# Performance work log

Hardware: AMD Instinct MI355X
Metric: run time of the kernel (lower is better)

## Reference

```python
import jax, jax.numpy as jnp
import numpy as np

N = 4096
IN_DIM = 256
OUT_DIM = 256
NUM_HEADS = 4
HEAD_DIM = OUT_DIM // NUM_HEADS


def setup_inputs() -> dict:
    key = jax.random.key(0)
    ks = jax.random.split(key, 10)
    x = jax.random.normal(ks[0], (N, IN_DIM), dtype=jnp.float32)
    adj = jax.random.randint(ks[1], (N, N), 0, 2, dtype=jnp.int32)
    adj = jnp.maximum(adj, jnp.eye(N, dtype=jnp.int32))  # self-loops -> no empty rows
    s_in = 1.0 / np.sqrt(IN_DIM)
    s_out = 1.0 / np.sqrt(OUT_DIM)
    Wq = jax.random.uniform(ks[2], (IN_DIM, OUT_DIM), jnp.float32, -s_in, s_in)
    bq = jnp.zeros((OUT_DIM,), jnp.float32)
    Wk = jax.random.uniform(ks[3], (IN_DIM, OUT_DIM), jnp.float32, -s_in, s_in)
    bk = jnp.zeros((OUT_DIM,), jnp.float32)
    Wv = jax.random.uniform(ks[4], (IN_DIM, OUT_DIM), jnp.float32, -s_in, s_in)
    bv = jnp.zeros((OUT_DIM,), jnp.float32)
    Wo = jax.random.uniform(ks[5], (OUT_DIM, OUT_DIM), jnp.float32, -s_out, s_out)
    bo = jnp.zeros((OUT_DIM,), jnp.float32)
    gamma = jnp.ones((OUT_DIM,), jnp.float32)
    beta = jnp.zeros((OUT_DIM,), jnp.float32)
    return {"x": x, "adj": adj, "Wq": Wq, "bq": bq, "Wk": Wk, "bk": bk,
            "Wv": Wv, "bv": bv, "Wo": Wo, "bo": bo, "gamma": gamma, "beta": beta}


def layer_norm(h, gamma, beta, eps=1e-5):
    mu = jnp.mean(h, axis=-1, keepdims=True)
    var = jnp.mean(jnp.square(h - mu), axis=-1, keepdims=True)
    return (h - mu) * jax.lax.rsqrt(var + eps) * gamma + beta


def reference(x, adj, Wq, bq, Wk, bk, Wv, bv, Wo, bo, gamma, beta):
    n = x.shape[0]
    q_proj = x @ Wq + bq                       # (N, out_dim), reused for residual
    Q = q_proj.reshape(n, NUM_HEADS, HEAD_DIM)
    K = (x @ Wk + bk).reshape(n, NUM_HEADS, HEAD_DIM)
    V = (x @ Wv + bv).reshape(n, NUM_HEADS, HEAD_DIM)
    scores = jnp.einsum('nhd,mhd->nmh', Q, K) / np.sqrt(HEAD_DIM)
    scores = jnp.where(adj[:, :, None] == 0, -jnp.inf, scores)
    attn = jax.nn.softmax(scores, axis=1)      # softmax over neighbor axis m
    out = jnp.einsum('nmh,mhd->nhd', attn, V).reshape(n, OUT_DIM)
    out = out @ Wo + bo
    return layer_norm(out + q_proj, gamma, beta)
```

## Files before the change

### kernel.cpp

```cpp
#include <hip/hip_runtime.h>
#include <math.h>

#define NN 4096
#define DIM 256
#define NHEADS 4
#define HDIM 64

typedef short bf16x8 __attribute__((ext_vector_type(8)));
typedef float f32x4  __attribute__((ext_vector_type(4)));

__device__ __forceinline__ unsigned short f2bf(float f) {
    unsigned int u = __float_as_uint(f);
    u += 0x7fffu + ((u >> 16) & 1u);
    return (unsigned short)(u >> 16);
}
__device__ __forceinline__ float bf2f(unsigned short h) {
    return __uint_as_float(((unsigned int)h) << 16);
}
__device__ __forceinline__ void async16(const void* g, void* l) {
    __builtin_amdgcn_global_load_lds(
        (const __attribute__((address_space(1))) unsigned int*)g,
        (__attribute__((address_space(3))) unsigned int*)l, 16, 0, 0);
}

__global__ __launch_bounds__(256)
void prep_kernel(const float* __restrict__ W0, const float* __restrict__ W1,
                 const float* __restrict__ W2, const float* __restrict__ W3,
                 unsigned short* __restrict__ T0, unsigned short* __restrict__ T1,
                 unsigned short* __restrict__ T2, unsigned short* __restrict__ T3)
{
    __shared__ unsigned short Ts[64][65];
    const int b = blockIdx.x, t = threadIdx.x;
    const int mat = b >> 4, tile = b & 15;
    const int r0 = (tile >> 2) * 64, c0 = (tile & 3) * 64;
    const float* W = (mat == 0) ? W0 : (mat == 1) ? W1 : (mat == 2) ? W2 : W3;
    unsigned short* T = (mat == 0) ? T0 : (mat == 1) ? T1 : (mat == 2) ? T2 : T3;
    {
        int r = t >> 2, c4 = (t & 3) * 16;
        #pragma unroll
        for (int j = 0; j < 4; ++j) {
            float4 v = *reinterpret_cast<const float4*>(W + (size_t)(r0 + r) * DIM + c0 + c4 + j * 4);
            Ts[c4 + j * 4 + 0][r] = f2bf(v.x);
            Ts[c4 + j * 4 + 1][r] = f2bf(v.y);
            Ts[c4 + j * 4 + 2][r] = f2bf(v.z);
            Ts[c4 + j * 4 + 3][r] = f2bf(v.w);
        }
    }
    __syncthreads();
    {
        int d = t >> 2, k4 = (t & 3) * 16;
        #pragma unroll
        for (int j = 0; j < 4; ++j) {
            ushort4 u;
            u.x = Ts[d][k4 + j * 4 + 0];
            u.y = Ts[d][k4 + j * 4 + 1];
            u.z = Ts[d][k4 + j * 4 + 2];
            u.w = Ts[d][k4 + j * 4 + 3];
            *reinterpret_cast<ushort4*>(T + (size_t)(c0 + d) * DIM + r0 + k4 + j * 4) = u;
        }
    }
}

__global__ __launch_bounds__(256)
void qkv_mask(const float* __restrict__ x,
              const unsigned short* __restrict__ WqT, const unsigned short* __restrict__ WkT,
              const unsigned short* __restrict__ WvT,
              const float* __restrict__ bq, const float* __restrict__ bk, const float* __restrict__ bv,
              unsigned short* __restrict__ Qo, unsigned short* __restrict__ Ko,
              unsigned short* __restrict__ VTo,
              const int* __restrict__ adj, unsigned long long* __restrict__ maskT)
{
    const int b = blockIdx.x, t = threadIdx.x, w = t >> 6, l = t & 63;

    if (b >= 384) {
        const int ww = (b - 384) * 4 + w;
        for (int idx = ww; idx < 65536; idx += 8192) {
            const int row = idx >> 4, st = idx & 15;
            const int* ap = adj + (size_t)row * NN + st * 256 + l;
            const int a0 = ap[0];
            const int a1 = ap[64];
            const int a2 = ap[128];
            const int a3 = ap[192];
            unsigned long long b0 = __ballot(a0 != 0);
            unsigned long long b1 = __ballot(a1 != 0);
            unsigned long long b2 = __ballot(a2 != 0);
            unsigned long long b3 = __ballot(a3 != 0);
            if (l < 4) {
                unsigned long long bb = (l == 0) ? b0 : (l == 1) ? b1 : (l == 2) ? b2 : b3;
                maskT[(size_t)row * 64 + st * 4 + l] = bb;
            }
        }
        return;
    }

    const int l15 = l & 15, lg = l >> 4;
    const int which = b >> 7, xb = b & 127;
    const int row0 = xb * 32 + (w >> 1) * 16;
    const int col0 = (w & 1) * 128;
    const unsigned short* WT; const float* bias;
    if (which == 0)      { WT = WqT; bias = bq; }
    else if (which == 1) { WT = WkT; bias = bk; }
    else                 { WT = WvT; bias = bv; }

    f32x4 acc[8] = {};
    for (int k0 = 0; k0 < DIM; k0 += 32) {
        const float* xp = x + (size_t)(row0 + l15) * DIM + k0 + lg * 8;
        float4 x0 = *reinterpret_cast<const float4*>(xp);
        float4 x1 = *reinterpret_cast<const float4*>(xp + 4);
        union { unsigned u[4]; bf16x8 v; } xa;
        asm("v_cvt_pk_bf16_f32 %0, %1, %2" : "=v"(xa.u[0]) : "v"(x0.x), "v"(x0.y));
        asm("v_cvt_pk_bf16_f32 %0, %1, %2" : "=v"(xa.u[1]) : "v"(x0.z), "v"(x0.w));
        asm("v_cvt_pk_bf16_f32 %0, %1, %2" : "=v"(xa.u[2]) : "v"(x1.x), "v"(x1.y));
        asm("v_cvt_pk_bf16_f32 %0, %1, %2" : "=v"(xa.u[3]) : "v"(x1.z), "v"(x1.w));
        #pragma unroll
        for (int nt = 0; nt < 8; ++nt) {
            bf16x8 wb = *(const bf16x8*)(WT + (size_t)(col0 + nt * 16 + l15) * DIM + k0 + lg * 8);
            acc[nt] = __builtin_amdgcn_mfma_f32_16x16x32_bf16(xa.v, wb, acc[nt], 0, 0, 0);
        }
    }
    #pragma unroll
    for (int nt = 0; nt < 8; ++nt) {
        int col = col0 + nt * 16 + l15;
        float bb = bias[col];
        #pragma unroll
        for (int r = 0; r < 4; ++r) {
            int row = row0 + lg * 4 + r;
            float ov = acc[nt][r] + bb;
            if (which == 1) ov *= 0.18033688f;
            unsigned short val = f2bf(ov);
            if (which == 2) {
                int rb = row & 63;
                int vnt = rb >> 4, vlg = (rb >> 2) & 3, vr = rb & 3;
                int pos = ((vnt & 1) << 5) | (vlg << 3) | ((vnt >> 1) << 2) | vr;
                VTo[(size_t)col * NN + ((row & ~63) | pos)] = val;
            } else if (which == 0) Qo[(size_t)row * DIM + col] = val;
            else                   Ko[(size_t)row * DIM + col] = val;
        }
    }
}

template<int NTILES>
__global__ __launch_bounds__(256, 8)
void attn_mfma(const unsigned short* __restrict__ Qb, const unsigned short* __restrict__ Kb,
               const unsigned short* __restrict__ VT, const unsigned long long* __restrict__ maskT,
               unsigned short* __restrict__ Opart, float* __restrict__ lpart)
{
    constexpr int NSTR = NTILES / 4;
    __shared__ unsigned short Kt[2][64][64];
    __shared__ unsigned short Vt[2][64][64];

    const int t = threadIdx.x, w = t >> 6, l = t & 63, l15 = l & 15, lg = l >> 4;
    const int bid = blockIdx.x;
    const int slice = (bid & 7) + 8 * (bid >> 9);
    const int qb    = (bid >> 3) & 63;
    const int h  = slice & 3;
    const int sp = slice >> 2;
    const int n0 = qb * 64;
    const int kv_base = sp * NTILES * 64;
    const int qrow = n0 + w * 16;

    const unsigned short* qp = Qb + (size_t)(qrow + l15) * DIM + h * HDIM + lg * 8;
    const bf16x8 qa0 = *(const bf16x8*)(qp);
    const bf16x8 qa1 = *(const bf16x8*)(qp + 32);

    const unsigned long long* mbase = maskT + (size_t)(qrow + l15) * 64 + (kv_base >> 6);

    const int srow  = w * 16 + (l >> 3);
    const int sunit = (l & 7) ^ (srow & 7);
    const unsigned short* kS = Kb + (size_t)(kv_base + srow) * DIM + h * HDIM + sunit * 8;
    const unsigned short* vS = VT + (size_t)(h * HDIM + srow) * NN + kv_base + sunit * 8;

    const int xr  = l15 & 7;
    const int ko0 = (lg ^ xr) << 4;
    const int ko1 = ((4 + lg) ^ xr) << 4;

    const short onev = (l15 == 0) ? (short)0x3F80 : (short)0;
    const bf16x8 onesb = {onev, onev, onev, onev, onev, onev, onev, onev};

    f32x4 oa[4] = {};
    f32x4 os = {};

    {
        unsigned short* kd = &Kt[0][w * 16][0];
        unsigned short* vd = &Vt[0][w * 16][0];
        async16(kS, kd); async16(kS + 8 * DIM, kd + 8 * 64);
        async16(vS, vd); async16(vS + 8 * NN,  vd + 8 * 64);
    }

    #pragma unroll 1
    for (int st = 0; st < NSTR; ++st) {
        const ulonglong4 m4 = *reinterpret_cast<const ulonglong4*>(mbase + st * 4);

        #pragma unroll
        for (int m = 0; m < 4; ++m) {
            const int tl = st * 4 + m;
            asm volatile("s_waitcnt vmcnt(0)" ::: "memory");
            __builtin_amdgcn_s_barrier();
            __builtin_amdgcn_sched_barrier(0);

            if (tl + 1 < NTILES) {
                const int bb = (tl + 1) & 1;
                unsigned short* kd = &Kt[bb][w * 16][0];
                unsigned short* vd = &Vt[bb][w * 16][0];
                const unsigned short* ks = kS + (size_t)(tl + 1) * 64 * DIM;
                const unsigned short* vs = vS + (tl + 1) * 64;
                async16(ks, kd); async16(ks + 8 * DIM, kd + 8 * 64);
                async16(vs, vd); async16(vs + 8 * NN,  vd + 8 * 64);
            }

            const int cb = tl & 1;
            const char* kbase = (const char*)&Kt[cb][0][0] + l15 * 128;
            const char* vbase = (const char*)&Vt[cb][0][0] + l15 * 128;

            f32x4 sa[4] = {};
            __builtin_amdgcn_s_setprio(1);
            #pragma unroll
            for (int nt = 0; nt < 4; ++nt) {
                bf16x8 kb0 = *(const bf16x8*)(kbase + nt * 2048 + ko0);
                bf16x8 kb1 = *(const bf16x8*)(kbase + nt * 2048 + ko1);
                sa[nt] = __builtin_amdgcn_mfma_f32_16x16x32_bf16(kb0, qa0, sa[nt], 0, 0, 0);
                sa[nt] = __builtin_amdgcn_mfma_f32_16x16x32_bf16(kb1, qa1, sa[nt], 0, 0, 0);
            }
            __builtin_amdgcn_s_setprio(0);

            const unsigned long long w64 =
                (m == 0) ? m4.x : (m == 1) ? m4.y : (m == 2) ? m4.z : m4.w;
            const unsigned long long sh = w64 >> (lg * 4);
            const unsigned shlo = (unsigned)sh, shhi = (unsigned)(sh >> 32);
            float p[4][4];
            #pragma unroll
            for (int nt = 0; nt < 4; ++nt) {
                #pragma unroll
                for (int r = 0; r < 4; ++r) {
                    const int bitpos = nt * 16 + r;
                    const unsigned word = (bitpos < 32) ? shlo : shhi;
                    const unsigned bit = (word >> (bitpos & 31)) & 1u;
                    p[nt][r] = exp2f(bit ? sa[nt][r] : -INFINITY);
                }
            }
            union { unsigned u[4]; bf16x8 v; } a0, a1;
            asm("v_cvt_pk_bf16_f32 %0, %1, %2" : "=v"(a0.u[0]) : "v"(p[0][0]), "v"(p[0][1]));
            asm("v_cvt_pk_bf16_f32 %0, %1, %2" : "=v"(a0.u[1]) : "v"(p[0][2]), "v"(p[0][3]));
            asm("v_cvt_pk_bf16_f32 %0, %1, %2" : "=v"(a0.u[2]) : "v"(p[2][0]), "v"(p[2][1]));
            asm("v_cvt_pk_bf16_f32 %0, %1, %2" : "=v"(a0.u[3]) : "v"(p[2][2]), "v"(p[2][3]));
            asm("v_cvt_pk_bf16_f32 %0, %1, %2" : "=v"(a1.u[0]) : "v"(p[1][0]), "v"(p[1][1]));
            asm("v_cvt_pk_bf16_f32 %0, %1, %2" : "=v"(a1.u[1]) : "v"(p[1][2]), "v"(p[1][3]));
            asm("v_cvt_pk_bf16_f32 %0, %1, %2" : "=v"(a1.u[2]) : "v"(p[3][0]), "v"(p[3][1]));
            asm("v_cvt_pk_bf16_f32 %0, %1, %2" : "=v"(a1.u[3]) : "v"(p[3][2]), "v"(p[3][3]));
            const bf16x8 pa0 = a0.v;
            const bf16x8 pa1 = a1.v;

            __builtin_amdgcn_s_setprio(1);
            #pragma unroll
            for (int nt = 0; nt < 4; ++nt) {
                bf16x8 vb0 = *(const bf16x8*)(vbase + nt * 2048 + ko0);
                bf16x8 vb1 = *(const bf16x8*)(vbase + nt * 2048 + ko1);
                oa[nt] = __builtin_amdgcn_mfma_f32_16x16x32_bf16(pa0, vb0, oa[nt], 0, 0, 0);
                oa[nt] = __builtin_amdgcn_mfma_f32_16x16x32_bf16(pa1, vb1, oa[nt], 0, 0, 0);
            }
            os = __builtin_amdgcn_mfma_f32_16x16x32_bf16(pa0, onesb, os, 0, 0, 0);
            os = __builtin_amdgcn_mfma_f32_16x16x32_bf16(pa1, onesb, os, 0, 0, 0);
            __builtin_amdgcn_s_setprio(0);
        }
    }

    #pragma unroll
    for (int r = 0; r < 4; ++r) {
        const int qr = qrow + lg * 4 + r;
        #pragma unroll
        for (int nt = 0; nt < 4; ++nt)
            Opart[((size_t)sp * NN + qr) * DIM + h * HDIM + nt * 16 + l15] = f2bf(oa[nt][r]);
        if (l15 == 0)
            lpart[((size_t)sp * NN + qr) * NHEADS + h] = os[r];
    }
}

__global__ __launch_bounds__(256)
void out_ln_fused(const unsigned short* __restrict__ Opart, const float* __restrict__ lpart,
                  const unsigned short* __restrict__ WoT, const float* __restrict__ bo,
                  const unsigned short* __restrict__ Rb, const float* __restrict__ gamma,
                  const float* __restrict__ beta, float* __restrict__ out, int S)
{
    __shared__ unsigned short As[16][264];
    __shared__ float redsum[4][16];
    __shared__ float redsq[4][16];
    const int t = threadIdx.x, w = t >> 6, l = t & 63, l15 = l & 15, lg = l >> 4;
    const int row0 = blockIdx.x * 16;

    {
        const int row = t >> 4;
        const int d0  = (t & 15) * 16;
        const int hh  = d0 >> 6;
        float lsum = 0.f;
        for (int s = 0; s < S; ++s)
            lsum += lpart[((size_t)s * NN + row0 + row) * NHEADS + hh];
        const float inv = 1.f / lsum;
        float a16[16] = {};
        for (int s = 0; s < S; ++s) {
            const unsigned short* op = Opart + ((size_t)s * NN + row0 + row) * DIM + d0;
            #pragma unroll
            for (int j4 = 0; j4 < 4; ++j4) {
                ushort4 u = *reinterpret_cast<const ushort4*>(op + j4 * 4);
                a16[j4 * 4 + 0] += bf2f(u.x);
                a16[j4 * 4 + 1] += bf2f(u.y);
                a16[j4 * 4 + 2] += bf2f(u.z);
                a16[j4 * 4 + 3] += bf2f(u.w);
            }
        }
        #pragma unroll
        for (int j4 = 0; j4 < 4; ++j4) {
            ushort4 ov;
            ov.x = f2bf(a16[j4 * 4 + 0] * inv);
            ov.y = f2bf(a16[j4 * 4 + 1] * inv);
            ov.z = f2bf(a16[j4 * 4 + 2] * inv);
            ov.w = f2bf(a16[j4 * 4 + 3] * inv);
            *reinterpret_cast<ushort4*>(&As[row][d0 + j4 * 4]) = ov;
        }
    }
    __syncthreads();

    const int col0 = w * 64;
    f32x4 acc[4] = {};
    for (int k0 = 0; k0 < DIM; k0 += 32) {
        bf16x8 xa = *reinterpret_cast<const bf16x8*>(&As[l15][k0 + lg * 8]);
        #pragma unroll
        for (int nt = 0; nt < 4; ++nt) {
            bf16x8 wb = *(const bf16x8*)(WoT + (size_t)(col0 + nt * 16 + l15) * DIM + k0 + lg * 8);
            acc[nt] = __builtin_amdgcn_mfma_f32_16x16x32_bf16(xa, wb, acc[nt], 0, 0, 0);
        }
    }

    float psum[4] = {0, 0, 0, 0}, psq[4] = {0, 0, 0, 0};
    #pragma unroll
    for (int nt = 0; nt < 4; ++nt) {
        int col = col0 + nt * 16 + l15;
        float bb = bo[col];
        #pragma unroll
        for (int r = 0; r < 4; ++r) {
            int row = row0 + lg * 4 + r;
            float xv = acc[nt][r] + bb + bf2f(Rb[(size_t)row * DIM + col]);
            acc[nt][r] = xv;
            psum[r] += xv; psq[r] += xv * xv;
        }
    }
    #pragma unroll
    for (int r = 0; r < 4; ++r) {
        float s = psum[r], q = psq[r];
        s += __shfl_xor(s, 1); q += __shfl_xor(q, 1);
        s += __shfl_xor(s, 2); q += __shfl_xor(q, 2);
        s += __shfl_xor(s, 4); q += __shfl_xor(q, 4);
        s += __shfl_xor(s, 8); q += __shfl_xor(q, 8);
        psum[r] = s; psq[r] = q;
    }
    if (l15 == 0) {
        #pragma unroll
        for (int r = 0; r < 4; ++r) {
            redsum[w][lg * 4 + r] = psum[r];
            redsq[w][lg * 4 + r]  = psq[r];
        }
    }
    __syncthreads();

    float msave[4], rsave[4];
    #pragma unroll
    for (int r = 0; r < 4; ++r) {
        int row = lg * 4 + r;
        float s = redsum[0][row] + redsum[1][row] + redsum[2][row] + redsum[3][row];
        float q = redsq[0][row] + redsq[1][row] + redsq[2][row] + redsq[3][row];
        float mean = s * (1.f / 256.f);
        float var  = q * (1.f / 256.f) - mean * mean;
        msave[r] = mean;
        rsave[r] = rsqrtf(var + 1e-5f);
    }
    #pragma unroll
    for (int nt = 0; nt < 4; ++nt) {
        int col = col0 + nt * 16 + l15;
        float g = gamma[col], bt = beta[col];
        #pragma unroll
        for (int r = 0; r < 4; ++r) {
            int row = row0 + lg * 4 + r;
            out[(size_t)row * DIM + col] = (acc[nt][r] - msave[r]) * rsave[r] * g + bt;
        }
    }
}

extern "C" void kernel_launch(void* const* d_in, const int* in_sizes, int n_in,
                              void* d_out, int out_size, void* d_ws, size_t ws_size,
                              hipStream_t stream) {
    const float* x     = (const float*)d_in[0];
    const int*   adj   = (const int*)  d_in[1];
    const float* Wq    = (const float*)d_in[2];
    const float* bq    = (const float*)d_in[3];
    const float* Wk    = (const float*)d_in[4];
    const float* bk    = (const float*)d_in[5];
    const float* Wv    = (const float*)d_in[6];
    const float* bv    = (const float*)d_in[7];
    const float* Wo    = (const float*)d_in[8];
    const float* bo    = (const float*)d_in[9];
    const float* gamma = (const float*)d_in[10];
    const float* beta  = (const float*)d_in[11];
    float* out = (float*)d_out;

    char* ws = (char*)d_ws;
    const size_t MB = 1u << 20;
    unsigned short*     Qb    = (unsigned short*)(ws + 0 * MB);
    unsigned short*     Kb    = (unsigned short*)(ws + 2 * MB);
    unsigned short*     VT    = (unsigned short*)(ws + 4 * MB);
    unsigned long long* maskT = (unsigned long long*)(ws + 6 * MB);
    unsigned short*     WqT   = (unsigned short*)(ws + 8 * MB);
    unsigned short*     WkT   = (unsigned short*)(ws + 8 * MB + 128 * 1024);
    unsigned short*     WvT   = (unsigned short*)(ws + 8 * MB + 256 * 1024);
    unsigned short*     WoT   = (unsigned short*)(ws + 8 * MB + 384 * 1024);
    float*              lpart = (float*)(ws + 10 * MB + 512 * 1024);
    unsigned short*     Opart = (unsigned short*)(ws + 11 * MB);

    const int S = (ws_size >= 27 * MB) ? 8 : 4;

    prep_kernel<<<64, 256, 0, stream>>>(Wq, Wk, Wv, Wo, WqT, WkT, WvT, WoT);

    qkv_mask<<<384 + 2048, 256, 0, stream>>>(
        x, WqT, WkT, WvT, bq, bk, bv, Qb, Kb, VT, adj, maskT);

    if (S == 8)
        attn_mfma<8><<<2048, 256, 0, stream>>>(Qb, Kb, VT, maskT, Opart, lpart);
    else
        attn_mfma<16><<<1024, 256, 0, stream>>>(Qb, Kb, VT, maskT, Opart, lpart);

    out_ln_fused<<<NN / 16, 256, 0, stream>>>(
        Opart, lpart, WoT, bo, Qb, gamma, beta, out, S);
}
```

Before: 85.06 us.

## Switch attention to 32x32x16 MFMA tiles with 128-query blocks

The attention kernel now processes 128 query rows per block (32 per wave) using 32x32x16 bf16 MFMAs instead of 16x16x32. This halves the grid and doubles reuse of each K/V LDS tile across queries. The P matrix is re-laid out between the two MFMA shapes with cross-half lane shuffles, the row-sum is computed with scalar adds instead of a ones-vector MFMA, and the V transpose drops its custom permutation. Larger accumulators raise register pressure, so launch bounds drop to 4 blocks per CU, which lowers occupancy.

```diff
diff --git a/kernel.cpp b/kernel.cpp
--- a/kernel.cpp
+++ b/kernel.cpp
@@ -6,8 +6,9 @@
 #define NHEADS 4
 #define HDIM 64
 
-typedef short bf16x8 __attribute__((ext_vector_type(8)));
-typedef float f32x4  __attribute__((ext_vector_type(4)));
+typedef short bf16x8  __attribute__((ext_vector_type(8)));
+typedef float f32x4   __attribute__((ext_vector_type(4)));
+typedef float f32x16  __attribute__((ext_vector_type(16)));
 
 __device__ __forceinline__ unsigned short f2bf(float f) {
     unsigned int u = __float_as_uint(f);
@@ -128,19 +129,15 @@
             float ov = acc[nt][r] + bb;
             if (which == 1) ov *= 0.18033688f;
             unsigned short val = f2bf(ov);
-            if (which == 2) {
-                int rb = row & 63;
-                int vnt = rb >> 4, vlg = (rb >> 2) & 3, vr = rb & 3;
-                int pos = ((vnt & 1) << 5) | (vlg << 3) | ((vnt >> 1) << 2) | vr;
-                VTo[(size_t)col * NN + ((row & ~63) | pos)] = val;
-            } else if (which == 0) Qo[(size_t)row * DIM + col] = val;
-            else                   Ko[(size_t)row * DIM + col] = val;
+            if (which == 2)      VTo[(size_t)col * NN + row] = val;
+            else if (which == 0) Qo[(size_t)row * DIM + col] = val;
+            else                 Ko[(size_t)row * DIM + col] = val;
         }
     }
 }
 
 template<int NTILES>
-__global__ __launch_bounds__(256, 8)
+__global__ __launch_bounds__(256, 4)
 void attn_mfma(const unsigned short* __restrict__ Qb, const unsigned short* __restrict__ Kb,
                const unsigned short* __restrict__ VT, const unsigned long long* __restrict__ maskT,
                unsigned short* __restrict__ Opart, float* __restrict__ lpart)
@@ -149,36 +146,40 @@
     __shared__ unsigned short Kt[2][64][64];
     __shared__ unsigned short Vt[2][64][64];
 
-    const int t = threadIdx.x, w = t >> 6, l = t & 63, l15 = l & 15, lg = l >> 4;
+    const int t = threadIdx.x, w = t >> 6, l = t & 63, l31 = l & 31, hi = l >> 5;
     const int bid = blockIdx.x;
-    const int slice = (bid & 7) + 8 * (bid >> 9);
-    const int qb    = (bid >> 3) & 63;
+    const int slice = (bid & 7) + 8 * (bid >> 8);
+    const int qb    = (bid >> 3) & 31;
     const int h  = slice & 3;
     const int sp = slice >> 2;
-    const int n0 = qb * 64;
     const int kv_base = sp * NTILES * 64;
-    const int qrow = n0 + w * 16;
-
-    const unsigned short* qp = Qb + (size_t)(qrow + l15) * DIM + h * HDIM + lg * 8;
-    const bf16x8 qa0 = *(const bf16x8*)(qp);
-    const bf16x8 qa1 = *(const bf16x8*)(qp + 32);
-
-    const unsigned long long* mbase = maskT + (size_t)(qrow + l15) * 64 + (kv_base >> 6);
+    const int qbase = qb * 128 + w * 32;
+    const int q = qbase + l31;
+
+    bf16x8 qf0, qf1, qf2, qf3;
+    {
+        const unsigned short* qp = Qb + (size_t)q * DIM + h * HDIM + hi * 8;
+        qf0 = *(const bf16x8*)(qp);
+        qf1 = *(const bf16x8*)(qp + 16);
+        qf2 = *(const bf16x8*)(qp + 32);
+        qf3 = *(const bf16x8*)(qp + 48);
+    }
+
+    const unsigned long long* mbase = maskT + (size_t)q * 64 + (kv_base >> 6);
 
     const int srow  = w * 16 + (l >> 3);
     const int sunit = (l & 7) ^ (srow & 7);
     const unsigned short* kS = Kb + (size_t)(kv_base + srow) * DIM + h * HDIM + sunit * 8;
     const unsigned short* vS = VT + (size_t)(h * HDIM + srow) * NN + kv_base + sunit * 8;
 
-    const int xr  = l15 & 7;
-    const int ko0 = (lg ^ xr) << 4;
-    const int ko1 = ((4 + lg) ^ xr) << 4;
-
-    const short onev = (l15 == 0) ? (short)0x3F80 : (short)0;
-    const bf16x8 onesb = {onev, onev, onev, onev, onev, onev, onev, onev};
-
-    f32x4 oa[4] = {};
-    f32x4 os = {};
+    const int x7 = l31 & 7;
+    const int ko0 = ((0 + hi) ^ x7) << 4;
+    const int ko1 = ((2 + hi) ^ x7) << 4;
+    const int ko2 = ((4 + hi) ^ x7) << 4;
+    const int ko3 = ((6 + hi) ^ x7) << 4;
+
+    f32x16 oacc0 = {}, oacc1 = {};
+    float lsum = 0.f;
 
     {
         unsigned short* kd = &Kt[0][w * 16][0];
@@ -209,69 +210,91 @@
             }
 
             const int cb = tl & 1;
-            const char* kbase = (const char*)&Kt[cb][0][0] + l15 * 128;
-            const char* vbase = (const char*)&Vt[cb][0][0] + l15 * 128;
-
-            f32x4 sa[4] = {};
+            const char* kbase = (const char*)&Kt[cb][0][0] + l31 * 128;
+            const char* vbase = (const char*)&Vt[cb][0][0] + l31 * 128;
+
+            f32x16 sacc0 = {}, sacc1 = {};
             __builtin_amdgcn_s_setprio(1);
-            #pragma unroll
-            for (int nt = 0; nt < 4; ++nt) {
-                bf16x8 kb0 = *(const bf16x8*)(kbase + nt * 2048 + ko0);
-                bf16x8 kb1 = *(const bf16x8*)(kbase + nt * 2048 + ko1);
-                sa[nt] = __builtin_amdgcn_mfma_f32_16x16x32_bf16(kb0, qa0, sa[nt], 0, 0, 0);
-                sa[nt] = __builtin_amdgcn_mfma_f32_16x16x32_bf16(kb1, qa1, sa[nt], 0, 0, 0);
+            {
+                bf16x8 a0 = *(const bf16x8*)(kbase + ko0);
+                bf16x8 b0 = *(const bf16x8*)(kbase + 4096 + ko0);
+                sacc0 = __builtin_amdgcn_mfma_f32_32x32x16_bf16(a0, qf0, sacc0, 0, 0, 0);
+                sacc1 = __builtin_amdgcn_mfma_f32_32x32x16_bf16(b0, qf0, sacc1, 0, 0, 0);
+                bf16x8 a1 = *(const bf16x8*)(kbase + ko1);
+                bf16x8 b1 = *(const bf16x8*)(kbase + 4096 + ko1);
+                sacc0 = __builtin_amdgcn_mfma_f32_32x32x16_bf16(a1, qf1, sacc0, 0, 0, 0);
+                sacc1 = __builtin_amdgcn_mfma_f32_32x32x16_bf16(b1, qf1, sacc1, 0, 0, 0);
+                bf16x8 a2 = *(const bf16x8*)(kbase + ko2);
+                bf16x8 b2 = *(const bf16x8*)(kbase + 4096 + ko2);
+                sacc0 = __builtin_amdgcn_mfma_f32_32x32x16_bf16(a2, qf2, sacc0, 0, 0, 0);
+                sacc1 = __builtin_amdgcn_mfma_f32_32x32x16_bf16(b2, qf2, sacc1, 0, 0, 0);
+                bf16x8 a3 = *(const bf16x8*)(kbase + ko3);
+                bf16x8 b3 = *(const bf16x8*)(kbase + 4096 + ko3);
+                sacc0 = __builtin_amdgcn_mfma_f32_32x32x16_bf16(a3, qf3, sacc0, 0, 0, 0);
+                sacc1 = __builtin_amdgcn_mfma_f32_32x32x16_bf16(b3, qf3, sacc1, 0, 0, 0);
             }
             __builtin_amdgcn_s_setprio(0);
 
             const unsigned long long w64 =
                 (m == 0) ? m4.x : (m == 1) ? m4.y : (m == 2) ? m4.z : m4.w;
-            const unsigned long long sh = w64 >> (lg * 4);
-            const unsigned shlo = (unsigned)sh, shhi = (unsigned)(sh >> 32);
-            float p[4][4];
+            const unsigned long long sh = w64 >> (hi * 4);
+            const unsigned bits01 = (unsigned)sh;
+            const unsigned bits23 = (unsigned)(sh >> 32);
+
             #pragma unroll
-            for (int nt = 0; nt < 4; ++nt) {
+            for (int half = 0; half < 2; ++half) {
+                const unsigned bits = half ? bits23 : bits01;
+                float p[16];
                 #pragma unroll
-                for (int r = 0; r < 4; ++r) {
-                    const int bitpos = nt * 16 + r;
-                    const unsigned word = (bitpos < 32) ? shlo : shhi;
-                    const unsigned bit = (word >> (bitpos & 31)) & 1u;
-                    p[nt][r] = exp2f(bit ? sa[nt][r] : -INFINITY);
+                for (int r = 0; r < 16; ++r) {
+                    const int pos = (r & 3) + 8 * (r >> 2);
+                    const unsigned bit = (bits >> pos) & 1u;
+                    const float sv = half ? sacc1[r] : sacc0[r];
+                    p[r] = exp2f(bit ? sv : -INFINITY);
+                }
+                lsum += (((p[0] + p[1]) + (p[2] + p[3])) + ((p[4] + p[5]) + (p[6] + p[7]))) +
+                        (((p[8] + p[9]) + (p[10] + p[11])) + ((p[12] + p[13]) + (p[14] + p[15])));
+
+                #pragma unroll
+                for (int sl = 0; sl < 2; ++sl) {
+                    const int rb = sl * 8;
+                    const int ko = half ? (sl ? ko3 : ko2) : (sl ? ko1 : ko0);
+                    unsigned pk01, pk23, pk45, pk67;
+                    asm("v_cvt_pk_bf16_f32 %0, %1, %2" : "=v"(pk01) : "v"(p[rb + 0]), "v"(p[rb + 1]));
+                    asm("v_cvt_pk_bf16_f32 %0, %1, %2" : "=v"(pk23) : "v"(p[rb + 2]), "v"(p[rb + 3]));
+                    asm("v_cvt_pk_bf16_f32 %0, %1, %2" : "=v"(pk45) : "v"(p[rb + 4]), "v"(p[rb + 5]));
+                    asm("v_cvt_pk_bf16_f32 %0, %1, %2" : "=v"(pk67) : "v"(p[rb + 6]), "v"(p[rb + 7]));
+                    const unsigned send0 = hi ? pk01 : pk45;
+                    const unsigned send1 = hi ? pk23 : pk67;
+                    const unsigned recv0 = (unsigned)__shfl_xor((int)send0, 32);
+                    const unsigned recv1 = (unsigned)__shfl_xor((int)send1, 32);
+                    union { unsigned u[4]; bf16x8 v; } pa;
+                    pa.u[0] = hi ? recv0 : pk01;
+                    pa.u[1] = hi ? recv1 : pk23;
+                    pa.u[2] = hi ? pk45 : recv0;
+                    pa.u[3] = hi ? pk67 : recv1;
+
+                    bf16x8 vb0 = *(const bf16x8*)(vbase + ko);
+                    bf16x8 vb1 = *(const bf16x8*)(vbase + 4096 + ko);
+                    __builtin_amdgcn_s_setprio(1);
+                    oacc0 = __builtin_amdgcn_mfma_f32_32x32x16_bf16(pa.v, vb0, oacc0, 0, 0, 0);
+                    oacc1 = __builtin_amdgcn_mfma_f32_32x32x16_bf16(pa.v, vb1, oacc1, 0, 0, 0);
+                    __builtin_amdgcn_s_setprio(0);
                 }
             }
-            union { unsigned u[4]; bf16x8 v; } a0, a1;
-            asm("v_cvt_pk_bf16_f32 %0, %1, %2" : "=v"(a0.u[0]) : "v"(p[0][0]), "v"(p[0][1]));
-            asm("v_cvt_pk_bf16_f32 %0, %1, %2" : "=v"(a0.u[1]) : "v"(p[0][2]), "v"(p[0][3]));
-            asm("v_cvt_pk_bf16_f32 %0, %1, %2" : "=v"(a0.u[2]) : "v"(p[2][0]), "v"(p[2][1]));
-            asm("v_cvt_pk_bf16_f32 %0, %1, %2" : "=v"(a0.u[3]) : "v"(p[2][2]), "v"(p[2][3]));
-            asm("v_cvt_pk_bf16_f32 %0, %1, %2" : "=v"(a1.u[0]) : "v"(p[1][0]), "v"(p[1][1]));
-            asm("v_cvt_pk_bf16_f32 %0, %1, %2" : "=v"(a1.u[1]) : "v"(p[1][2]), "v"(p[1][3]));
-            asm("v_cvt_pk_bf16_f32 %0, %1, %2" : "=v"(a1.u[2]) : "v"(p[3][0]), "v"(p[3][1]));
-            asm("v_cvt_pk_bf16_f32 %0, %1, %2" : "=v"(a1.u[3]) : "v"(p[3][2]), "v"(p[3][3]));
-            const bf16x8 pa0 = a0.v;
-            const bf16x8 pa1 = a1.v;
-
-            __builtin_amdgcn_s_setprio(1);
-            #pragma unroll
-            for (int nt = 0; nt < 4; ++nt) {
-                bf16x8 vb0 = *(const bf16x8*)(vbase + nt * 2048 + ko0);
-                bf16x8 vb1 = *(const bf16x8*)(vbase + nt * 2048 + ko1);
-                oa[nt] = __builtin_amdgcn_mfma_f32_16x16x32_bf16(pa0, vb0, oa[nt], 0, 0, 0);
-                oa[nt] = __builtin_amdgcn_mfma_f32_16x16x32_bf16(pa1, vb1, oa[nt], 0, 0, 0);
-            }
-            os = __builtin_amdgcn_mfma_f32_16x16x32_bf16(pa0, onesb, os, 0, 0, 0);
-            os = __builtin_amdgcn_mfma_f32_16x16x32_bf16(pa1, onesb, os, 0, 0, 0);
-            __builtin_amdgcn_s_setprio(0);
-        }
-    }
-
-    #pragma unroll
-    for (int r = 0; r < 4; ++r) {
-        const int qr = qrow + lg * 4 + r;
-        #pragma unroll
-        for (int nt = 0; nt < 4; ++nt)
-            Opart[((size_t)sp * NN + qr) * DIM + h * HDIM + nt * 16 + l15] = f2bf(oa[nt][r]);
-        if (l15 == 0)
-            lpart[((size_t)sp * NN + qr) * NHEADS + h] = os[r];
+            __builtin_amdgcn_sched_barrier(0);
+        }
+    }
+
+    lsum += __shfl_xor(lsum, 32);
+    if (hi == 0)
+        lpart[((size_t)sp * NN + q) * NHEADS + h] = lsum;
+
+    #pragma unroll
+    for (int r = 0; r < 16; ++r) {
+        const int qr = qbase + (r & 3) + 8 * (r >> 2) + 4 * hi;
+        Opart[((size_t)sp * NN + qr) * DIM + h * HDIM + l31]      = f2bf(oacc0[r]);
+        Opart[((size_t)sp * NN + qr) * DIM + h * HDIM + 32 + l31] = f2bf(oacc1[r]);
     }
 }
 
@@ -345,12 +368,12 @@
     }
     #pragma unroll
     for (int r = 0; r < 4; ++r) {
-        float s = psum[r], q = psq[r];
-        s += __shfl_xor(s, 1); q += __shfl_xor(q, 1);
-        s += __shfl_xor(s, 2); q += __shfl_xor(q, 2);
-        s += __shfl_xor(s, 4); q += __shfl_xor(q, 4);
-        s += __shfl_xor(s, 8); q += __shfl_xor(q, 8);
-        psum[r] = s; psq[r] = q;
+        float s = psum[r], qq = psq[r];
+        s += __shfl_xor(s, 1); qq += __shfl_xor(qq, 1);
+        s += __shfl_xor(s, 2); qq += __shfl_xor(qq, 2);
+        s += __shfl_xor(s, 4); qq += __shfl_xor(qq, 4);
+        s += __shfl_xor(s, 8); qq += __shfl_xor(qq, 8);
+        psum[r] = s; psq[r] = qq;
     }
     if (l15 == 0) {
         #pragma unroll
@@ -366,9 +389,9 @@
     for (int r = 0; r < 4; ++r) {
         int row = lg * 4 + r;
         float s = redsum[0][row] + redsum[1][row] + redsum[2][row] + redsum[3][row];
-        float q = redsq[0][row] + redsq[1][row] + redsq[2][row] + redsq[3][row];
+        float qq = redsq[0][row] + redsq[1][row] + redsq[2][row] + redsq[3][row];
         float mean = s * (1.f / 256.f);
-        float var  = q * (1.f / 256.f) - mean * mean;
+        float var  = qq * (1.f / 256.f) - mean * mean;
         msave[r] = mean;
         rsave[r] = rsqrtf(var + 1e-5f);
     }
@@ -422,9 +445,9 @@
         x, WqT, WkT, WvT, bq, bk, bv, Qb, Kb, VT, adj, maskT);
 
     if (S == 8)
-        attn_mfma<8><<<2048, 256, 0, stream>>>(Qb, Kb, VT, maskT, Opart, lpart);
+        attn_mfma<8><<<1024, 256, 0, stream>>>(Qb, Kb, VT, maskT, Opart, lpart);
     else
-        attn_mfma<16><<<1024, 256, 0, stream>>>(Qb, Kb, VT, maskT, Opart, lpart);
+        attn_mfma<16><<<512, 256, 0, stream>>>(Qb, Kb, VT, maskT, Opart, lpart);
 
     out_ln_fused<<<NN / 16, 256, 0, stream>>>(
         Opart, lpart, WoT, bo, Qb, gamma, beta, out, S);
```

After: 112.0 us. 1.32x slower.
